# Performance work log

Hardware: AMD Instinct MI355X
Metric: run time of the kernel (lower is better)

The kernel has to match this reference:

```python
import jax, jax.numpy as jnp
import numpy as np

HIDDEN = 1024
NUM_HEADS = 16
DK = 64  # key_and_query_dim
DV = 64  # value_dim
NEG_INF = -1.0e9


def setup_inputs() -> dict:
    key = jax.random.key(0)
    ks = jax.random.split(key, 12)
    B, S = 4, 2048
    scale = 0.02
    return {
        "q_hidden_inputs": jax.random.normal(ks[0], (B, S, HIDDEN), dtype=jnp.float32),
        "k_hidden_inputs": jax.random.normal(ks[1], (B, S, HIDDEN), dtype=jnp.float32),
        "v_hidden_inputs": jax.random.normal(ks[2], (B, S, HIDDEN), dtype=jnp.float32),
        "mask": jax.random.randint(ks[3], (B, S, S), 0, 2) > 0,
        # per-head projection weights, stacked over heads: [H, hidden, dk/dv]
        "wq": jax.random.normal(ks[4], (NUM_HEADS, HIDDEN, DK), dtype=jnp.float32) * scale,
        "bq": jax.random.normal(ks[5], (NUM_HEADS, DK), dtype=jnp.float32) * scale,
        "wk": jax.random.normal(ks[6], (NUM_HEADS, HIDDEN, DK), dtype=jnp.float32) * scale,
        "bk": jax.random.normal(ks[7], (NUM_HEADS, DK), dtype=jnp.float32) * scale,
        "wv": jax.random.normal(ks[8], (NUM_HEADS, HIDDEN, DV), dtype=jnp.float32) * scale,
        "bv": jax.random.normal(ks[9], (NUM_HEADS, DV), dtype=jnp.float32) * scale,
        # output projection: [H*dv, hidden]
        "wo": jax.random.normal(ks[10], (NUM_HEADS * DV, HIDDEN), dtype=jnp.float32) * scale,
        "bo": jax.random.normal(ks[11], (HIDDEN,), dtype=jnp.float32) * scale,
    }


def reference(q_hidden_inputs, k_hidden_inputs, v_hidden_inputs, mask,
              wq, bq, wk, bk, wv, bv, wo, bo):
    # Per-head linear projections, vectorized over heads: [B, H, S, dk]
    q = jnp.einsum('bsd,hdk->bhsk', q_hidden_inputs, wq) + bq[None, :, None, :]
    k = jnp.einsum('bsd,hdk->bhsk', k_hidden_inputs, wk) + bk[None, :, None, :]
    v = jnp.einsum('bsd,hdv->bhsv', v_hidden_inputs, wv) + bv[None, :, None, :]
    # scores: [B, H, Sq, Sk]
    scores = jnp.einsum('bhsk,bhtk->bhst', q, k) / jnp.sqrt(jnp.float32(DK))
    scores = jnp.where(mask[:, None, :, :], scores, NEG_INF)
    attn = jax.nn.softmax(scores, axis=-1)
    out = jnp.einsum('bhst,bhtv->bhsv', attn, v)  # [B, H, Sq, dv]
    B, H, Sq, Dv = out.shape
    # heads concatenated along last dim in head order (same as torch.cat)
    out = jnp.transpose(out, (0, 2, 1, 3)).reshape(B, Sq, H * Dv)
    return out @ wo + bo
```

## Files before the change

### kernel.cpp

```cpp
#include <hip/hip_runtime.h>
#include <stdint.h>


typedef __bf16 bf16x8_t __attribute__((ext_vector_type(8)));
typedef float f32x4_t __attribute__((ext_vector_type(4)));
typedef short s16x4_t __attribute__((ext_vector_type(4)));

#define HID   1024
#define SLEN  2048
#define BATCH 4
#define NH    16
#define MROWS 8192
#define L2E   1.44269504f

__device__ __forceinline__ unsigned short bfbits(float f) {
  union { __bf16 h; unsigned short u; } v; v.h = (__bf16)f; return v.u;
}
__device__ __forceinline__ unsigned int packbf(float a, float b) {
  return (unsigned int)bfbits(a) | ((unsigned int)bfbits(b) << 16);
}
__device__ __forceinline__ float fast_exp2(float x) {
#if __has_builtin(__builtin_amdgcn_exp2f)
  return __builtin_amdgcn_exp2f(x);
#else
  return __exp2f(x);
#endif
}

__device__ __forceinline__ f32x4_t mfma16x16(s16x4_t a, s16x4_t b, f32x4_t c) {
#if __has_builtin(__builtin_amdgcn_mfma_f32_16x16x16bf16_1k)
  return __builtin_amdgcn_mfma_f32_16x16x16bf16_1k(a, b, c, 0, 0, 0);
#else
  asm("v_mfma_f32_16x16x16_bf16 %0, %1, %2, %0" : "+v"(c) : "v"(a), "v"(b));
  return c;
#endif
}

__device__ __forceinline__ void gload_lds16(const void* g, void* l) {
  __builtin_amdgcn_global_load_lds((const __attribute__((address_space(1))) void*)g,
                                   (__attribute__((address_space(3))) void*)l,
                                   16, 0, 0);
}

__device__ __forceinline__ bf16x8_t frag_ld(const unsigned short* lds, int row, int sblk) {
  int sp = sblk ^ (row & 7);
  return *(const bf16x8_t*)(lds + (row << 6) + (sp << 3));
}

__global__ void detect_mask_kernel(const unsigned int* __restrict__ m,
                                   unsigned int* __restrict__ flag) {
  unsigned int v = m[threadIdx.x];
  unsigned long long b = __ballot(v > 1u);
  if (threadIdx.x == 0) flag[0] = 0u;
  __syncthreads();
  if ((threadIdx.x & 63) == 0 && b) atomicOr(flag, 1u);
}

__global__ __launch_bounds__(256) void mask_bits_kernel(const void* __restrict__ maskp,
    const unsigned int* __restrict__ flag, unsigned long long* __restrict__ bits) {
  int lane = threadIdx.x & 63, wv = threadIdx.x >> 6;
  bool bytemask = flag[0] != 0u;
  size_t w0 = (size_t)blockIdx.x * 64 + (size_t)wv * 16;
  for (int it = 0; it < 16; ++it) {
    size_t word = w0 + it;
    unsigned int v;
    if (bytemask) v = ((const unsigned char*)maskp)[word * 64 + lane];
    else          v = ((const unsigned int*)maskp)[word * 64 + lane];
    unsigned long long bm = __ballot(v != 0u);
    if (lane == 0) bits[word] = bm;
  }
}

__global__ __launch_bounds__(256) void cvt_x_kernel(const float* __restrict__ src,
                                                    unsigned short* __restrict__ xb) {
  size_t base = (size_t)blockIdx.x * 1024 + (size_t)threadIdx.x * 4;
  float4 v = *(const float4*)(src + base);
  ushort4 o;
  o.x = bfbits(v.x); o.y = bfbits(v.y); o.z = bfbits(v.z); o.w = bfbits(v.w);
  *(ushort4*)(xb + base) = o;
}

__global__ __launch_bounds__(256) void pack_w_kernel(const float* __restrict__ wq,
    const float* __restrict__ wk, const float* __restrict__ wv,
    const float* __restrict__ wo, unsigned short* __restrict__ wt) {
  int z = blockIdx.y;
  int id = blockIdx.x * 256 + threadIdx.x;
  int n = id >> 8;
  int d0 = (id & 255) << 2;
  ushort4 o;
  if (z < 3) {
    const float* w = z == 0 ? wq : (z == 1 ? wk : wv);
    const float* base = w + (size_t)(n >> 6) * (HID * 64) + (n & 63);
    o.x = bfbits(base[(size_t)(d0 + 0) * 64]);
    o.y = bfbits(base[(size_t)(d0 + 1) * 64]);
    o.z = bfbits(base[(size_t)(d0 + 2) * 64]);
    o.w = bfbits(base[(size_t)(d0 + 3) * 64]);
  } else {
    o.x = bfbits(wo[(size_t)(d0 + 0) * HID + n]);
    o.y = bfbits(wo[(size_t)(d0 + 1) * HID + n]);
    o.z = bfbits(wo[(size_t)(d0 + 2) * HID + n]);
    o.w = bfbits(wo[(size_t)(d0 + 3) * HID + n]);
  }
  *(ushort4*)(wt + (size_t)z * (HID * HID) + (size_t)n * HID + d0) = o;
}

__device__ __forceinline__ void gemm_stage(const unsigned short* __restrict__ A,
    const unsigned short* __restrict__ B, unsigned short* la, unsigned short* lb,
    int tid, int w, int kt) {
#pragma unroll
  for (int i = 0; i < 4; ++i) {
    int flat = i * 256 + tid;
    int row = flat >> 3;
    int sl = (flat & 7) ^ (row & 7);
    gload_lds16(A + (size_t)row * HID + kt + sl * 8, la + ((i * 256 + w * 64) << 3));
    gload_lds16(B + (size_t)row * HID + kt + sl * 8, lb + ((i * 256 + w * 64) << 3));
  }
}

__device__ __forceinline__ void gemm_tile_mainloop(const unsigned short* __restrict__ A,
    const unsigned short* __restrict__ B, unsigned short (*lA)[128 * 64],
    unsigned short (*lB)[128 * 64], int tid, f32x4_t (&acc)[4][4]) {
  int lane = tid & 63, w = tid >> 6;
  int wr = (w >> 1) << 6, wc = (w & 1) << 6;
  gemm_stage(A, B, lA[0], lB[0], tid, w, 0);
  __syncthreads();
  int cur = 0;
  for (int kt = 0; kt < HID; kt += 64) {
    if (kt + 64 < HID)
      gemm_stage(A, B, lA[cur ^ 1], lB[cur ^ 1], tid, w, kt + 64);
    const unsigned short* la = lA[cur];
    const unsigned short* lb = lB[cur];
#pragma unroll
    for (int kk = 0; kk < 2; ++kk) {
      bf16x8_t af[4], bfr[4];
#pragma unroll
      for (int mi = 0; mi < 4; ++mi)
        af[mi] = frag_ld(la, wr + mi * 16 + (lane & 15), kk * 4 + (lane >> 4));
#pragma unroll
      for (int ni = 0; ni < 4; ++ni)
        bfr[ni] = frag_ld(lb, wc + ni * 16 + (lane & 15), kk * 4 + (lane >> 4));
#pragma unroll
      for (int mi = 0; mi < 4; ++mi)
#pragma unroll
        for (int ni = 0; ni < 4; ++ni)
          acc[mi][ni] = __builtin_amdgcn_mfma_f32_16x16x32_bf16(af[mi], bfr[ni],
                                                                acc[mi][ni], 0, 0, 0);
    }
    __syncthreads();
    cur ^= 1;
  }
}

__global__ __launch_bounds__(256) void gemm_qkv_kernel(
    const unsigned short* __restrict__ Ain, const unsigned short* __restrict__ Bin,
    const float* __restrict__ bias, unsigned short* __restrict__ Out, float scale) {
  __shared__ __align__(16) unsigned short lA[2][128 * 64];
  __shared__ __align__(16) unsigned short lB[2][128 * 64];
  int m0 = blockIdx.x * 128, n0 = blockIdx.y * 128;
  const unsigned short* A = Ain + (size_t)m0 * HID;
  const unsigned short* B = Bin + (size_t)n0 * HID;
  f32x4_t acc[4][4] = {};
  int tid = threadIdx.x;
  gemm_tile_mainloop(A, B, lA, lB, tid, acc);
  int lane = tid & 63, w = tid >> 6;
  int wr = (w >> 1) << 6, wc = (w & 1) << 6;
#pragma unroll
  for (int mi = 0; mi < 4; ++mi)
#pragma unroll
    for (int ni = 0; ni < 4; ++ni) {
      int col = n0 + wc + ni * 16 + (lane & 15);
      float bb = bias[col];
      int h = col >> 6, d = col & 63;
#pragma unroll
      for (int r = 0; r < 4; ++r) {
        int row = m0 + wr + mi * 16 + ((lane >> 4) << 2) + r;
        int b = row >> 11, s = row & 2047;
        Out[((((size_t)b * NH + h) * SLEN + s) << 6) + d] = bfbits((acc[mi][ni][r] + bb) * scale);
      }
    }
}

__global__ __launch_bounds__(256) void gemm_out_kernel(
    const unsigned short* __restrict__ Ob, const unsigned short* __restrict__ WoT,
    const float* __restrict__ bo, float* __restrict__ out) {
  __shared__ __align__(16) unsigned short lA[2][128 * 64];
  __shared__ __align__(16) unsigned short lB[2][128 * 64];
  int m0 = blockIdx.x * 128, n0 = blockIdx.y * 128;
  const unsigned short* A = Ob + (size_t)m0 * HID;
  const unsigned short* B = WoT + (size_t)n0 * HID;
  f32x4_t acc[4][4] = {};
  int tid = threadIdx.x;
  gemm_tile_mainloop(A, B, lA, lB, tid, acc);
  int lane = tid & 63, w = tid >> 6;
  int wr = (w >> 1) << 6, wc = (w & 1) << 6;
#pragma unroll
  for (int mi = 0; mi < 4; ++mi)
#pragma unroll
    for (int ni = 0; ni < 4; ++ni) {
      int col = n0 + wc + ni * 16 + (lane & 15);
      float bb = bo[col];
#pragma unroll
      for (int r = 0; r < 4; ++r) {
        int row = m0 + wr + mi * 16 + ((lane >> 4) << 2) + r;
        out[(size_t)row * HID + col] = acc[mi][ni][r] + bb;
      }
    }
}

__global__ __launch_bounds__(256) void attn_kernel(
    const unsigned short* __restrict__ Q, const unsigned short* __restrict__ K,
    const unsigned short* __restrict__ V, const unsigned long long* __restrict__ mbits,
    unsigned short* __restrict__ O) {
  __shared__ __align__(16) unsigned short lK[2][64 * 64];
  __shared__ __align__(16) unsigned short lV[2][64 * 64];
  int tid = threadIdx.x, lane = tid & 63, w = tid >> 6;
  int g = lane >> 4, ql = lane & 15;
  int bid = blockIdx.x;
  int bh = (bid & 7) * 8 + ((bid >> 3) >> 4);
  int qt = (bid >> 3) & 15;
  int b = bh >> 4, h = bh & 15;
  int q0 = qt * 128;
  const unsigned short* Qb = Q + (size_t)bh * (SLEN * 64);
  const unsigned short* Kb = K + (size_t)bh * (SLEN * 64);
  const unsigned short* Vb = V + (size_t)bh * (SLEN * 64);
  const unsigned long long* Mrow = mbits + (size_t)b * SLEN * 32;

  int kvp = tid >> 3;
  int dv0 = (tid & 7) << 3;

  int vbyte0 = (ql << 7) + (((g >> 1) ^ (ql & 7)) << 4) + ((g & 1) << 3);

  bf16x8_t qf[2][2];
#pragma unroll
  for (int mi = 0; mi < 2; ++mi)
#pragma unroll
    for (int kk = 0; kk < 2; ++kk) {
      int row = q0 + w * 32 + mi * 16 + ql;
      qf[mi][kk] = *(const bf16x8_t*)(Qb + (size_t)row * 64 + kk * 32 + g * 8);
    }

  s16x4_t ones4 = {0x3F80, 0x3F80, 0x3F80, 0x3F80};

  f32x4_t aco[2][4] = {};
  f32x4_t slacc[2] = {};

#pragma unroll
  for (int i = 0; i < 2; ++i) {
    int flat = i * 256 + tid;
    int row = flat >> 3;
    int sl = (flat & 7) ^ (row & 7);
    gload_lds16(Kb + (size_t)row * 64 + sl * 8, lK[0] + ((i * 256 + w * 64) << 3));
  }
  {
    const unsigned short* vs = Vb + (size_t)(kvp * 2) * 64 + dv0;
    bf16x8_t v0 = *(const bf16x8_t*)(vs);
    bf16x8_t v1 = *(const bf16x8_t*)(vs + 64);
    union { __bf16 b[8]; unsigned short u[8]; } a0, a1;
    *(bf16x8_t*)a0.b = v0; *(bf16x8_t*)a1.b = v1;
#pragma unroll
    for (int e = 0; e < 8; ++e) {
      int dv = dv0 + e;
      unsigned int val = (unsigned int)a0.u[e] | ((unsigned int)a1.u[e] << 16);
      int sp2 = (kvp >> 2) ^ (dv & 7);
      *(unsigned int*)((char*)lV[0] + dv * 128 + sp2 * 16 + (kvp & 3) * 4) = val;
    }
  }
  __syncthreads();

  int cur = 0;
  for (int kt = 0; kt < SLEN / 64; ++kt) {
    bf16x8_t vn0, vn1;
    bool pre = (kt + 1) < SLEN / 64;
    if (pre) {
#pragma unroll
      for (int i = 0; i < 2; ++i) {
        int flat = i * 256 + tid;
        int row = flat >> 3;
        int sl = (flat & 7) ^ (row & 7);
        gload_lds16(Kb + (size_t)((kt + 1) * 64 + row) * 64 + sl * 8,
                    lK[cur ^ 1] + ((i * 256 + w * 64) << 3));
      }
      const unsigned short* vs = Vb + (size_t)((kt + 1) * 64 + kvp * 2) * 64 + dv0;
      vn0 = *(const bf16x8_t*)(vs);
      vn1 = *(const bf16x8_t*)(vs + 64);
    }

    unsigned long long bg[2];
#pragma unroll
    for (int mi = 0; mi < 2; ++mi)
      bg[mi] = Mrow[(size_t)(q0 + w * 32 + mi * 16 + ql) * 32 + kt] >> (4 * g);

    const unsigned short* kbuf = lK[cur];
    const unsigned short* vbuf = lV[cur];
    f32x4_t st[2][4];
#pragma unroll
    for (int mi = 0; mi < 2; ++mi)
#pragma unroll
      for (int ni = 0; ni < 4; ++ni) st[mi][ni] = (f32x4_t){0.f, 0.f, 0.f, 0.f};
#pragma unroll
    for (int kk = 0; kk < 2; ++kk) {
      bf16x8_t kf[4];
#pragma unroll
      for (int ni = 0; ni < 4; ++ni)
        kf[ni] = frag_ld(kbuf, ni * 16 + ql, kk * 4 + g);
#pragma unroll
      for (int mi = 0; mi < 2; ++mi)
#pragma unroll
        for (int ni = 0; ni < 4; ++ni)
          st[mi][ni] = __builtin_amdgcn_mfma_f32_16x16x32_bf16(kf[ni], qf[mi][kk],
                                                               st[mi][ni], 0, 0, 0);
    }

    unsigned int pb[2][4][2];
#pragma unroll
    for (int mi = 0; mi < 2; ++mi)
#pragma unroll
      for (int ni = 0; ni < 4; ++ni) {
        float p[4];
#pragma unroll
        for (int r = 0; r < 4; ++r) {
          float e = fast_exp2(st[mi][ni][r]);
          p[r] = ((unsigned int)(bg[mi] >> (16 * ni + r)) & 1u) ? e : 0.f;
        }
        pb[mi][ni][0] = packbf(p[0], p[1]);
        pb[mi][ni][1] = packbf(p[2], p[3]);
      }

#pragma unroll
    for (int c = 0; c < 4; ++c) {
      s16x4_t vfa[4];
#pragma unroll
      for (int dvf = 0; dvf < 4; ++dvf) {
        union { uint2 u; s16x4_t s; } t;
        t.u = *(const uint2*)((const char*)vbuf + ((vbyte0 ^ (c << 5)) + dvf * 2048));
        vfa[dvf] = t.s;
      }
#pragma unroll
      for (int mi = 0; mi < 2; ++mi) {
        union { unsigned int u[2]; s16x4_t s; } pp;
        pp.u[0] = pb[mi][c][0]; pp.u[1] = pb[mi][c][1];
        slacc[mi] = mfma16x16(ones4, pp.s, slacc[mi]);
#pragma unroll
        for (int dvf = 0; dvf < 4; ++dvf)
          aco[mi][dvf] = mfma16x16(vfa[dvf], pp.s, aco[mi][dvf]);
      }
    }

    if (pre) {
      union { __bf16 b[8]; unsigned short u[8]; } a0, a1;
      *(bf16x8_t*)a0.b = vn0; *(bf16x8_t*)a1.b = vn1;
#pragma unroll
      for (int e = 0; e < 8; ++e) {
        int dv = dv0 + e;
        unsigned int val = (unsigned int)a0.u[e] | ((unsigned int)a1.u[e] << 16);
        int sp2 = (kvp >> 2) ^ (dv & 7);
        *(unsigned int*)((char*)lV[cur ^ 1] + dv * 128 + sp2 * 16 + (kvp & 3) * 4) = val;
      }
    }
    __syncthreads();
    cur ^= 1;
  }

  unsigned short* eb = (unsigned short*)lK;
#pragma unroll
  for (int mi = 0; mi < 2; ++mi) {
    float inv = 1.0f / slacc[mi][0];
    int prow = w * 32 + mi * 16 + ql;
#pragma unroll
    for (int dvf = 0; dvf < 4; ++dvf) {
      unsigned int lo = packbf(aco[mi][dvf][0] * inv, aco[mi][dvf][1] * inv);
      unsigned int hi = packbf(aco[mi][dvf][2] * inv, aco[mi][dvf][3] * inv);
      int sl = (2 * dvf + (g >> 1)) ^ (prow & 7);
      *(uint2*)((char*)eb + prow * 128 + sl * 16 + (g & 1) * 8) = make_uint2(lo, hi);
    }
  }
#pragma unroll
  for (int it = 0; it < 8; ++it) {
    int rloc = g + 4 * it;
    int row = w * 32 + rloc;
    int sl = (ql >> 1) ^ (row & 7);
    uint2 v = *(const uint2*)((const char*)eb + row * 128 + sl * 16 + (ql & 1) * 8);
    int qrow = q0 + row;
    *(uint2*)(O + (((size_t)b * SLEN + qrow) << 10) + h * 64 + ql * 4) = v;
  }
}

extern "C" void kernel_launch(void* const* d_in, const int* in_sizes, int n_in,
                              void* d_out, int out_size, void* d_ws, size_t ws_size,
                              hipStream_t stream) {
  (void)in_sizes; (void)n_in; (void)out_size; (void)ws_size;
  const float* xq = (const float*)d_in[0];
  const float* xk = (const float*)d_in[1];
  const float* xv = (const float*)d_in[2];
  const void*  mask = d_in[3];
  const float* wq = (const float*)d_in[4];
  const float* bq = (const float*)d_in[5];
  const float* wk = (const float*)d_in[6];
  const float* bk = (const float*)d_in[7];
  const float* wv = (const float*)d_in[8];
  const float* bv = (const float*)d_in[9];
  const float* wo = (const float*)d_in[10];
  const float* bo = (const float*)d_in[11];
  float* out = (float*)d_out;

  char* ws = (char*)d_ws;
  unsigned short* XbZ  = (unsigned short*)(ws);
  unsigned short* Ob   = (unsigned short*)(ws);
  unsigned short* Wt   = (unsigned short*)(ws + 16777216ull);
  unsigned short* QKV  = (unsigned short*)(ws + 25165824ull);
  unsigned int*   flag = (unsigned int*)(ws + 75497472ull);
  unsigned long long* mbits = (unsigned long long*)d_out;

  const float* xs[3]   = {xq, xk, xv};
  const float* bias[3] = {bq, bk, bv};

  detect_mask_kernel<<<1, 256, 0, stream>>>((const unsigned int*)mask, flag);
  mask_bits_kernel<<<4096, 256, 0, stream>>>(mask, flag, mbits);
  pack_w_kernel<<<dim3(1024, 4), 256, 0, stream>>>(wq, wk, wv, wo, Wt);
  for (int z = 0; z < 3; ++z) {
    cvt_x_kernel<<<8192, 256, 0, stream>>>(xs[z], XbZ);
    gemm_qkv_kernel<<<dim3(64, 8), 256, 0, stream>>>(
        XbZ, Wt + (size_t)z * (HID * HID), bias[z],
        QKV + (size_t)z * ((size_t)MROWS * 1024), z == 0 ? 0.125f * L2E : 1.0f);
  }
  attn_kernel<<<1024, 256, 0, stream>>>(QKV, QKV + 8388608ull,
                                        QKV + 16777216ull, mbits, Ob);
  gemm_out_kernel<<<dim3(64, 8), 256, 0, stream>>>(Ob, Wt + 3ull * (HID * HID), bo, out);
}
```

Measured before the change: 305.8 us.

## Pre-transpose V in a separate kernel and stream K/V via direct LDS loads

Adds a kernel that writes V transposed and swizzled into scratch space inside the output buffer. The attention kernel can then fetch both K and V tiles with async global-to-LDS loads, replacing the per-iteration register load and scattered LDS transpose stores for V. It also hoists address arithmetic into incrementing pointers, splits the mask word into 32-bit halves, and raises wave priority around the MFMA sections. The cost is an extra kernel launch plus a full read and write of V, and the scratch region inside d_out must not overlap live data.

```diff
diff --git a/kernel.cpp b/kernel.cpp
--- a/kernel.cpp
+++ b/kernel.cpp
@@ -104,6 +104,36 @@
   *(ushort4*)(wt + (size_t)z * (HID * HID) + (size_t)n * HID + d0) = o;
 }
 
+__global__ __launch_bounds__(256) void transpose_v_kernel(
+    const unsigned short* __restrict__ V, unsigned short* __restrict__ VT) {
+  __shared__ unsigned int t[64 * 32];
+  int tid = threadIdx.x;
+  int bh = blockIdx.y;
+  int s0 = blockIdx.x * 64;
+  const unsigned short* Vb = V + (size_t)bh * (SLEN * 64);
+  int sp = tid >> 3, d0 = (tid & 7) << 3;
+  const unsigned short* vs = Vb + (size_t)(s0 + sp * 2) * 64 + d0;
+  bf16x8_t v0 = *(const bf16x8_t*)(vs);
+  bf16x8_t v1 = *(const bf16x8_t*)(vs + 64);
+  union { __bf16 b[8]; unsigned short u[8]; } a0, a1;
+  *(bf16x8_t*)a0.b = v0; *(bf16x8_t*)a1.b = v1;
+#pragma unroll
+  for (int e = 0; e < 8; ++e) {
+    int d = d0 + e;
+    unsigned int val = (unsigned int)a0.u[e] | ((unsigned int)a1.u[e] << 16);
+    int slot = (sp >> 2) ^ (d & 7);
+    t[d * 32 + slot * 4 + (sp & 3)] = val;
+  }
+  __syncthreads();
+#pragma unroll
+  for (int it = 0; it < 2; ++it) {
+    int gid = it * 256 + tid;
+    int d = gid >> 3, slot = gid & 7;
+    uint4 vv = *(const uint4*)(t + d * 32 + ((slot ^ (d & 7)) << 2));
+    *(uint4*)(VT + (size_t)bh * (64 * SLEN) + (size_t)d * SLEN + s0 + slot * 8) = vv;
+  }
+}
+
 __device__ __forceinline__ void gemm_stage(const unsigned short* __restrict__ A,
     const unsigned short* __restrict__ B, unsigned short* la, unsigned short* lb,
     int tid, int w, int kt) {
@@ -209,7 +239,7 @@
 
 __global__ __launch_bounds__(256) void attn_kernel(
     const unsigned short* __restrict__ Q, const unsigned short* __restrict__ K,
-    const unsigned short* __restrict__ V, const unsigned long long* __restrict__ mbits,
+    const unsigned short* __restrict__ VT, const unsigned long long* __restrict__ mbits,
     unsigned short* __restrict__ O) {
   __shared__ __align__(16) unsigned short lK[2][64 * 64];
   __shared__ __align__(16) unsigned short lV[2][64 * 64];
@@ -221,12 +251,18 @@
   int b = bh >> 4, h = bh & 15;
   int q0 = qt * 128;
   const unsigned short* Qb = Q + (size_t)bh * (SLEN * 64);
-  const unsigned short* Kb = K + (size_t)bh * (SLEN * 64);
-  const unsigned short* Vb = V + (size_t)bh * (SLEN * 64);
-  const unsigned long long* Mrow = mbits + (size_t)b * SLEN * 32;
-
-  int kvp = tid >> 3;
-  int dv0 = (tid & 7) << 3;
+
+  int f0 = tid, f1 = 256 + tid;
+  int r0 = f0 >> 3, r1 = f1 >> 3;
+  int s0 = (f0 & 7) ^ (r0 & 7), s1 = (f1 & 7) ^ (r1 & 7);
+  const unsigned short* kS0 = K + (size_t)bh * (SLEN * 64) + (size_t)r0 * 64 + s0 * 8;
+  const unsigned short* kS1 = K + (size_t)bh * (SLEN * 64) + (size_t)r1 * 64 + s1 * 8;
+  const unsigned short* vS0 = VT + (size_t)bh * (64 * SLEN) + (size_t)r0 * SLEN + s0 * 8;
+  const unsigned short* vS1 = VT + (size_t)bh * (64 * SLEN) + (size_t)r1 * SLEN + s1 * 8;
+  int d0off = (0 * 256 + w * 64) << 3;
+  int d1off = (1 * 256 + w * 64) << 3;
+  const unsigned long long* mp0 = mbits + ((size_t)b * SLEN + (q0 + w * 32 + ql)) * 32;
+  const unsigned long long* mp1 = mp0 + 16 * 32;
 
   int vbyte0 = (ql << 7) + (((g >> 1) ^ (ql & 7)) << 4) + ((g & 1) << 3);
 
@@ -244,51 +280,27 @@
   f32x4_t aco[2][4] = {};
   f32x4_t slacc[2] = {};
 
-#pragma unroll
-  for (int i = 0; i < 2; ++i) {
-    int flat = i * 256 + tid;
-    int row = flat >> 3;
-    int sl = (flat & 7) ^ (row & 7);
-    gload_lds16(Kb + (size_t)row * 64 + sl * 8, lK[0] + ((i * 256 + w * 64) << 3));
-  }
-  {
-    const unsigned short* vs = Vb + (size_t)(kvp * 2) * 64 + dv0;
-    bf16x8_t v0 = *(const bf16x8_t*)(vs);
-    bf16x8_t v1 = *(const bf16x8_t*)(vs + 64);
-    union { __bf16 b[8]; unsigned short u[8]; } a0, a1;
-    *(bf16x8_t*)a0.b = v0; *(bf16x8_t*)a1.b = v1;
-#pragma unroll
-    for (int e = 0; e < 8; ++e) {
-      int dv = dv0 + e;
-      unsigned int val = (unsigned int)a0.u[e] | ((unsigned int)a1.u[e] << 16);
-      int sp2 = (kvp >> 2) ^ (dv & 7);
-      *(unsigned int*)((char*)lV[0] + dv * 128 + sp2 * 16 + (kvp & 3) * 4) = val;
-    }
-  }
+  gload_lds16(kS0, (unsigned short*)lK[0] + d0off);
+  gload_lds16(kS1, (unsigned short*)lK[0] + d1off);
+  gload_lds16(vS0, (unsigned short*)lV[0] + d0off);
+  gload_lds16(vS1, (unsigned short*)lV[0] + d1off);
+  kS0 += 4096; kS1 += 4096; vS0 += 64; vS1 += 64;
   __syncthreads();
 
   int cur = 0;
   for (int kt = 0; kt < SLEN / 64; ++kt) {
-    bf16x8_t vn0, vn1;
-    bool pre = (kt + 1) < SLEN / 64;
-    if (pre) {
-#pragma unroll
-      for (int i = 0; i < 2; ++i) {
-        int flat = i * 256 + tid;
-        int row = flat >> 3;
-        int sl = (flat & 7) ^ (row & 7);
-        gload_lds16(Kb + (size_t)((kt + 1) * 64 + row) * 64 + sl * 8,
-                    lK[cur ^ 1] + ((i * 256 + w * 64) << 3));
-      }
-      const unsigned short* vs = Vb + (size_t)((kt + 1) * 64 + kvp * 2) * 64 + dv0;
-      vn0 = *(const bf16x8_t*)(vs);
-      vn1 = *(const bf16x8_t*)(vs + 64);
-    }
-
-    unsigned long long bg[2];
-#pragma unroll
-    for (int mi = 0; mi < 2; ++mi)
-      bg[mi] = Mrow[(size_t)(q0 + w * 32 + mi * 16 + ql) * 32 + kt] >> (4 * g);
+    if (kt + 1 < SLEN / 64) {
+      unsigned short* kn = (unsigned short*)lK[cur ^ 1];
+      unsigned short* vn = (unsigned short*)lV[cur ^ 1];
+      gload_lds16(kS0, kn + d0off);
+      gload_lds16(kS1, kn + d1off);
+      gload_lds16(vS0, vn + d0off);
+      gload_lds16(vS1, vn + d1off);
+      kS0 += 4096; kS1 += 4096; vS0 += 64; vS1 += 64;
+    }
+
+    unsigned long long bg0 = mp0[kt] >> (4 * g);
+    unsigned long long bg1 = mp1[kt] >> (4 * g);
 
     const unsigned short* kbuf = lK[cur];
     const unsigned short* vbuf = lV[cur];
@@ -297,6 +309,7 @@
     for (int mi = 0; mi < 2; ++mi)
 #pragma unroll
       for (int ni = 0; ni < 4; ++ni) st[mi][ni] = (f32x4_t){0.f, 0.f, 0.f, 0.f};
+    __builtin_amdgcn_s_setprio(1);
 #pragma unroll
     for (int kk = 0; kk < 2; ++kk) {
       bf16x8_t kf[4];
@@ -310,22 +323,30 @@
           st[mi][ni] = __builtin_amdgcn_mfma_f32_16x16x32_bf16(kf[ni], qf[mi][kk],
                                                                st[mi][ni], 0, 0, 0);
     }
+    __builtin_amdgcn_s_setprio(0);
 
     unsigned int pb[2][4][2];
 #pragma unroll
-    for (int mi = 0; mi < 2; ++mi)
+    for (int mi = 0; mi < 2; ++mi) {
+      unsigned long long bgs = mi ? bg1 : bg0;
+      unsigned int mw0 = (unsigned int)bgs;
+      unsigned int mw1 = (unsigned int)(bgs >> 32);
 #pragma unroll
       for (int ni = 0; ni < 4; ++ni) {
+        unsigned int mword = (ni < 2) ? mw0 : mw1;
+        int base = (ni & 1) * 16;
         float p[4];
 #pragma unroll
         for (int r = 0; r < 4; ++r) {
           float e = fast_exp2(st[mi][ni][r]);
-          p[r] = ((unsigned int)(bg[mi] >> (16 * ni + r)) & 1u) ? e : 0.f;
+          p[r] = ((mword >> (base + r)) & 1u) ? e : 0.f;
         }
         pb[mi][ni][0] = packbf(p[0], p[1]);
         pb[mi][ni][1] = packbf(p[2], p[3]);
       }
-
+    }
+
+    __builtin_amdgcn_s_setprio(1);
 #pragma unroll
     for (int c = 0; c < 4; ++c) {
       s16x4_t vfa[4];
@@ -345,18 +366,8 @@
           aco[mi][dvf] = mfma16x16(vfa[dvf], pp.s, aco[mi][dvf]);
       }
     }
-
-    if (pre) {
-      union { __bf16 b[8]; unsigned short u[8]; } a0, a1;
-      *(bf16x8_t*)a0.b = vn0; *(bf16x8_t*)a1.b = vn1;
-#pragma unroll
-      for (int e = 0; e < 8; ++e) {
-        int dv = dv0 + e;
-        unsigned int val = (unsigned int)a0.u[e] | ((unsigned int)a1.u[e] << 16);
-        int sp2 = (kvp >> 2) ^ (dv & 7);
-        *(unsigned int*)((char*)lV[cur ^ 1] + dv * 128 + sp2 * 16 + (kvp & 3) * 4) = val;
-      }
-    }
+    __builtin_amdgcn_s_setprio(0);
+
     __syncthreads();
     cur ^= 1;
   }
@@ -410,6 +421,7 @@
   unsigned short* QKV  = (unsigned short*)(ws + 25165824ull);
   unsigned int*   flag = (unsigned int*)(ws + 75497472ull);
   unsigned long long* mbits = (unsigned long long*)d_out;
+  unsigned short* VTp = (unsigned short*)((char*)d_out + 2097152ull);
 
   const float* xs[3]   = {xq, xk, xv};
   const float* bias[3] = {bq, bk, bv};
@@ -423,7 +435,7 @@
         XbZ, Wt + (size_t)z * (HID * HID), bias[z],
         QKV + (size_t)z * ((size_t)MROWS * 1024), z == 0 ? 0.125f * L2E : 1.0f);
   }
-  attn_kernel<<<1024, 256, 0, stream>>>(QKV, QKV + 8388608ull,
-                                        QKV + 16777216ull, mbits, Ob);
+  transpose_v_kernel<<<dim3(32, 64), 256, 0, stream>>>(QKV + 16777216ull, VTp);
+  attn_kernel<<<1024, 256, 0, stream>>>(QKV, QKV + 8388608ull, VTp, mbits, Ob);
   gemm_out_kernel<<<dim3(64, 8), 256, 0, stream>>>(Ob, Wt + 3ull * (HID * HID), bo, out);
 }
```

Result: no change. 300.6 us, median of 2 (-1.7%).
